# Performance work log

Hardware: AMD Instinct MI355X
Metric: run time of the kernel (lower is better)

The kernel has to match this reference:

```python
import jax, jax.numpy as jnp
import numpy as np

FRONT, END = 1, 2            # COMBINE_FRONT / COMBINE_END label values
BOS_ID, EOS_ID = 0, 1
BS, SLEN, D, H, L = 16, 256, 1024, 16, 2
N_POS = 512                  # N_MAX_POSITIONS


def setup_inputs():
    key = jax.random.key(0)
    ks = iter(jax.random.split(key, 80))
    nrm = lambda shape: jax.random.normal(next(ks), shape, dtype=jnp.float32) * 0.02
    inp = {}
    inp["encoded"] = jax.random.normal(next(ks), (BS, SLEN, D), dtype=jnp.float32)
    inp["lengths"] = jnp.full((BS,), SLEN, dtype=jnp.int32)  # assert slen == lengths.max()
    # deterministic valid word-span labels: [F,F,F,E,O,F,E,O] repeated -> words of 4 and 2 subwords
    pat = np.tile(np.array([1, 1, 1, 2, 0, 1, 2, 0], dtype=np.int32), SLEN // 8)
    inp["combine_labels"] = jnp.asarray(np.broadcast_to(pat, (BS, SLEN)).copy())
    inp["lang_id"] = 0
    inp["pos_emb"] = nrm((N_POS, D))
    inp["special_emb"] = nrm((3, D)).at[2].set(0.0)  # padding_idx=2 row zeroed
    for p in ("ctx", "wc"):
        for w in ("Wq", "Wk", "Wv", "Wo"):
            inp[p + "_" + w] = nrm((L, D, D))
        for b in ("bq", "bk", "bv", "bo", "b2", "be1", "be2"):
            inp[p + "_" + b] = jnp.zeros((L, D), dtype=jnp.float32)
        inp[p + "_W1"] = nrm((L, D, 4 * D))
        inp[p + "_b1"] = jnp.zeros((L, 4 * D), dtype=jnp.float32)
        inp[p + "_W2"] = nrm((L, 4 * D, D))
        inp[p + "_g1"] = jnp.ones((L, D), dtype=jnp.float32)
        inp[p + "_g2"] = jnp.ones((L, D), dtype=jnp.float32)
    return inp


def _ln(x, g, b):
    m = x.mean(-1, keepdims=True)
    v = ((x - m) ** 2).mean(-1, keepdims=True)
    return (x - m) / jnp.sqrt(v + 1e-5) * g + b


def _encoder(x, pad, P):
    # post-norm TransformerEncoder (torch default): attn -> add&LN -> relu-FFN -> add&LN
    Wq, Wk, Wv, Wo, bq, bk, bv, bo, W1, b1, W2, b2, g1, be1, g2, be2 = P
    B, S, Dm = x.shape
    hd = Dm // H
    scale = 1.0 / np.sqrt(hd)
    for i in range(Wq.shape[0]):
        q = (x @ Wq[i] + bq[i]).reshape(B, S, H, hd)
        k = (x @ Wk[i] + bk[i]).reshape(B, S, H, hd)
        v = (x @ Wv[i] + bv[i]).reshape(B, S, H, hd)
        s = jnp.einsum("bqhd,bkhd->bhqk", q, k) * scale
        s = jnp.where(pad[:, None, None, :], -1e9, s)  # src_key_padding_mask
        a = jax.nn.softmax(s, axis=-1)
        o = jnp.einsum("bhqk,bkhd->bqhd", a, v).reshape(B, S, Dm) @ Wo[i] + bo[i]
        x = _ln(x + o, g1[i], be1[i])
        h = jax.nn.relu(x @ W1[i] + b1[i]) @ W2[i] + b2[i]
        x = _ln(x + h, g2[i], be2[i])
    return x


def _word_inputs(encoded, combine_labels, special_emb):
    # vectorized replacement of the nested python-loop ragged span builder;
    # index math on the (concrete) labels in numpy, gathers/scatters in jnp.
    cl = np.asarray(combine_labels)
    f = cl == FRONT
    e = cl == END
    c = np.cumsum(f.astype(np.int64), axis=1)
    frontrun = c - np.maximum.accumulate(np.where(f, 0, c), axis=1)  # run of FRONTs ending here
    fr_prev = np.pad(frontrun[:, :-1], ((0, 0), (1, 0)))
    slot = np.where(f, frontrun, fr_prev + 1)  # 1-based slot inside word (slot 0 = BOS)
    e_flat = e.reshape(-1)
    wid = np.cumsum(e_flat) - e_flat  # word id = #ENDs strictly before, row-major order
    tok_idx = np.nonzero((f | e).reshape(-1))[0]
    w_tok = wid[tok_idx]
    s_tok = slot.reshape(-1)[tok_idx]
    wlen = fr_prev[e] + 3  # k subwords (fr_prev+1) + BOS + EOS
    n_word = wlen.shape[0]
    maxL = int(wlen.max())
    Dm = encoded.shape[-1]
    x = jnp.zeros((n_word, maxL, Dm), dtype=encoded.dtype)
    x = x.at[:, 0].set(special_emb[BOS_ID])
    x = x.at[np.arange(n_word), wlen - 1].set(special_emb[EOS_ID])  # eos at slot k+1
    x = x.at[w_tok, s_tok].set(encoded.reshape(-1, Dm)[tok_idx])
    return x, wlen


def _forward(encoded, lengths, combine_labels, pos_emb, special_emb, ctx, wc):
    S = encoded.shape[1]
    pad = jnp.asarray(np.arange(S)[None, :] >= np.asarray(lengths)[:, None])
    x = _encoder(encoded + pos_emb[:S][None], pad, ctx)          # another_encode
    winp, wlen = _word_inputs(x, combine_labels, special_emb)    # ragged gather, [n_word, maxL, D]
    maxL = winp.shape[1]
    wpad = jnp.asarray(np.arange(maxL)[None, :] >= wlen[:, None])
    y = _encoder(winp + pos_emb[:maxL][None], wpad, wc)          # word_encode
    return y[:, 0]  # position-0 (BOS) representation, [n_word, D]


def reference(encoded, lengths, combine_labels, lang_id, pos_emb, special_emb,
              ctx_Wq, ctx_Wk, ctx_Wv, ctx_Wo, ctx_bq, ctx_bk, ctx_bv, ctx_bo,
              ctx_W1, ctx_b1, ctx_W2, ctx_b2, ctx_g1, ctx_be1, ctx_g2, ctx_be2,
              wc_Wq, wc_Wk, wc_Wv, wc_Wo, wc_bq, wc_bk, wc_bv, wc_bo,
              wc_W1, wc_b1, wc_W2, wc_b2, wc_g1, wc_be1, wc_g2, wc_be2):
    ctx = (ctx_Wq, ctx_Wk, ctx_Wv, ctx_Wo, ctx_bq, ctx_bk, ctx_bv, ctx_bo,
           ctx_W1, ctx_b1, ctx_W2, ctx_b2, ctx_g1, ctx_be1, ctx_g2, ctx_be2)
    wc = (wc_Wq, wc_Wk, wc_Wv, wc_Wo, wc_bq, wc_bk, wc_bv, wc_bo,
          wc_W1, wc_b1, wc_W2, wc_b2, wc_g1, wc_be1, wc_g2, wc_be2)
    return _forward(encoded, lengths, combine_labels, pos_emb, special_emb, ctx, wc)
```

## Files before the change

kernel.cpp:

```cpp
#include <hip/hip_runtime.h>
#include <stdint.h>

typedef unsigned short u16;
typedef __attribute__((ext_vector_type(8))) short short8;
typedef __attribute__((ext_vector_type(4))) short short4v;
typedef __attribute__((ext_vector_type(4))) float f32x4;

#define DEV static __device__ __forceinline__

constexpr int B = 16, S = 256, D = 1024, H = 16, LYR = 2, FF = 4096;
constexpr int Mc = B * S;
constexpr int MAXL = 6;
constexpr int QKVS = 3 * D;

DEV u16 f2b(float f) {
  union { float f; uint32_t u; } a; a.f = f;
  uint32_t r = a.u + 0x7fffu + ((a.u >> 16) & 1u);
  return (u16)(r >> 16);
}
DEV float b2f(u16 b) {
  union { uint32_t u; float f; } a; a.u = ((uint32_t)b) << 16;
  return a.f;
}

DEV void glds16(const u16* g, u16* l) {
  __builtin_amdgcn_global_load_lds((const __attribute__((address_space(1))) void*)g,
                                   (__attribute__((address_space(3))) void*)l, 16, 0, 0);
}

struct TBatch {
  const float* src[6];
  u16* dst[6];
  int Kd[6];
  int Nd[6];
  int base[6];
};

__global__ __launch_bounds__(256) void transpose_batch(TBatch tb, int unused) {
  __shared__ float tile[64][65];
  const int bid = blockIdx.x;
  int wi = 0;
#pragma unroll
  for (int i = 1; i < 6; i++)
    if (bid >= tb.base[i]) wi = i;
  const float* __restrict__ W = tb.src[wi];
  u16* __restrict__ Wt = tb.dst[wi];
  const int K = tb.Kd[wi], N = tb.Nd[wi];
  const int local = bid - tb.base[wi];
  const int ntx = N >> 6;
  const int bn = (local % ntx) * 64, bk = (local / ntx) * 64;
  const int t = threadIdx.x;
  const int lr = t >> 2, lc = (t & 3) * 16;
#pragma unroll
  for (int q = 0; q < 4; q++) {
    float4 v = *(const float4*)&W[(size_t)(bk + lr) * N + bn + lc + q * 4];
    *(float4*)&tile[lr][lc + q * 4] = v;
  }
  __syncthreads();
  const int k0 = (t & 7) * 8;
#pragma unroll
  for (int p = 0; p < 2; p++) {
    const int n = (t >> 3) + p * 32;
    short8 o;
#pragma unroll
    for (int j = 0; j < 8; j++) o[j] = (short)f2b(tile[k0 + j][n]);
    *(short8*)&Wt[(size_t)(bn + n) * K + bk + k0] = o;
  }
}


template <int PASSES>
DEV void stage_rows(const u16* P, int lda, int k0, u16* Dst, int t) {
#pragma unroll
  for (int p = 0; p < PASSES; p++)
    glds16(P + (size_t)(p * 32) * lda + k0, Dst + p * 2048 + t * 8);
}

DEV void compute_tile(const u16* Asb, const u16* Bsb, f32x4 (&acc)[4][8],
                      int wm, int wn, int li, int hi) {
#pragma unroll
  for (int ks = 0; ks < 2; ks++) {
    const int ch = ((((ks << 2) | hi) ^ (li & 7)) * 8);
    short8 af[4], bfr[8];
#pragma unroll
    for (int i = 0; i < 4; i++)
      af[i] = *(const short8*)&Asb[(wm + i * 16 + li) * 64 + ch];
#pragma unroll
    for (int j = 0; j < 8; j++)
      bfr[j] = *(const short8*)&Bsb[(wn + j * 16 + li) * 64 + ch];
#pragma unroll
    for (int i = 0; i < 4; i++)
#pragma unroll
      for (int j = 0; j < 8; j++)
        acc[i][j] = __builtin_amdgcn_mfma_f32_16x16x32_bf16(af[i], bfr[j], acc[i][j], 0, 0, 0);
  }
}

template <int EPI, bool SPLITB, bool SPLITK>
__global__ __launch_bounds__(256, 2) void gemm_bt(const u16* __restrict__ A,
                                                  const u16* __restrict__ Bt,
                                                  const float* __restrict__ bias0,
                                                  const float* __restrict__ bias1,
                                                  const float* __restrict__ bias2,
                                                  float* __restrict__ Cf, u16* __restrict__ Cb,
                                                  int M, int N, int K, int lda, int NB) {
  __shared__ u16 As[128 * 64];
  __shared__ u16 Bs[256 * 64];
  const int t = threadIdx.x, lane = t & 63, w = t >> 6;
  const int wm = (w >> 1) * 64, wn = (w & 1) * 128;
  const int nwg = gridDim.x;
  const int cpx = nwg >> 3;
  const int swz = (blockIdx.x & 7) * cpx + (blockIdx.x >> 3);
  int sblk = 0, rem = swz;
  if (SPLITK) {
    const int tps = nwg >> 1;
    sblk = (swz >= tps) ? 1 : 0;
    rem = swz - sblk * tps;
  }
  const int n0 = (rem % NB) * 256, m0 = (rem / NB) * 128;
  const int pr = t >> 3;
  const int scb = (((t & 7) ^ (pr & 7)) * 8);
  f32x4 acc[4][8] = {};
  const u16* Ap = A + (size_t)sblk * K + (size_t)(m0 + pr) * lda + scb;
  const u16* Bp = Bt + (size_t)sblk * K + (size_t)(n0 + pr) * lda + scb;
  const int li = lane & 15, hi = lane >> 4;

  for (int k0 = 0; k0 < K; k0 += 64) {
    stage_rows<4>(Ap, lda, k0, &As[0], t);
    stage_rows<8>(Bp, lda, k0, &Bs[0], t);
    __syncthreads();
    compute_tile(&As[0], &Bs[0], acc, wm, wn, li, hi);
    __syncthreads();
  }

  u16* Cbs = Cb;
  if (SPLITK && EPI == 3) Cbs = Cb + (size_t)sblk * M * N;
  const int rg = hi * 4;
#pragma unroll
  for (int j = 0; j < 8; j++) {
    const int col = n0 + wn + j * 16 + li;
    float bv = 0.f;
    if (EPI != 3)
      bv = SPLITB ? (col < 1024 ? bias0 : col < 2048 ? bias1 : bias2)[col & 1023]
                  : bias0[col];
#pragma unroll
    for (int i = 0; i < 4; i++) {
      const int row0 = m0 + wm + i * 16 + rg;
#pragma unroll
      for (int r = 0; r < 4; r++) {
        float v = acc[i][j][r] + bv;
        if (EPI == 2) v = fmaxf(v, 0.f);
        if (EPI == 0) Cf[(size_t)(row0 + r) * N + col] = v;
        else Cbs[(size_t)(row0 + r) * N + col] = f2b(v);
      }
    }
  }
}

__global__ __launch_bounds__(256) void transpose_v(const u16* __restrict__ QKV,
                                                   u16* __restrict__ Vt) {
  const int kb = blockIdx.x, h = blockIdx.y, b = blockIdx.z;
  __shared__ u16 tile[64][72];
  const int t = threadIdx.x, lr = t >> 3, lc = (t & 7) * 8;
#pragma unroll
  for (int p = 0; p < 2; p++) {
    int r = lr + p * 32;
    *(short8*)&tile[r][lc] =
        *(const short8*)&QKV[(size_t)(b * 256 + kb * 64 + r) * QKVS + 2048 + h * 64 + lc];
  }
  __syncthreads();
#pragma unroll
  for (int p = 0; p < 2; p++) {
    int hd = lr + p * 32;
    short8 v8;
#pragma unroll
    for (int j = 0; j < 8; j++) v8[j] = (short)tile[lc + j][hd];
    *(short8*)&Vt[(size_t)((b * 16 + h) * 64 + hd) * 256 + kb * 64 + lc] = v8;
  }
}

__global__ __launch_bounds__(256) void attn_ctx(const u16* __restrict__ QKV,
                                                const u16* __restrict__ Vt,
                                                u16* __restrict__ AO,
                                                const int* __restrict__ lengths) {
  const int qt = blockIdx.x, h = blockIdx.y, b = blockIdx.z;
  __shared__ u16 Qs[64 * 64], Ks[64 * 64], Vs[64 * 64], Ps[64 * 64];
  const int t = threadIdx.x, lane = t & 63, w = t >> 6;
  const int len = lengths[b];
  const bool full = (len >= 256);
  const int lr = t >> 3, lc = (t & 7) * 8;
#pragma unroll
  for (int p = 0; p < 2; p++) {
    int r = lr + p * 32;
    *(short8*)&Qs[r * 64 + lc] =
        *(const short8*)&QKV[(size_t)(b * 256 + qt * 64 + r) * QKVS + h * 64 + lc];
  }
  const int li = lane & 15, kk = (lane >> 4) * 8, rg = (lane >> 4) * 4;
  float mrun[4], lrun[4];
  f32x4 oacc[4] = {};
#pragma unroll
  for (int r = 0; r < 4; r++) { mrun[r] = -1e30f; lrun[r] = 0.f; }

  for (int kt = 0; kt < 4; kt++) {
    __syncthreads();
#pragma unroll
    for (int p = 0; p < 2; p++) {
      int r = lr + p * 32;
      *(short8*)&Ks[r * 64 + lc] =
          *(const short8*)&QKV[(size_t)(b * 256 + kt * 64 + r) * QKVS + 1024 + h * 64 + lc];
      *(short8*)&Vs[r * 64 + lc] =
          *(const short8*)&Vt[(size_t)((b * 16 + h) * 64 + r) * 256 + kt * 64 + lc];
    }
    __syncthreads();
    f32x4 s[4] = {};
    short8 aq0 = *(const short8*)&Qs[(w * 16 + li) * 64 + kk];
    short8 aq1 = *(const short8*)&Qs[(w * 16 + li) * 64 + 32 + kk];
    __builtin_amdgcn_s_setprio(1);
#pragma unroll
    for (int fn = 0; fn < 4; fn++) {
      short8 b0 = *(const short8*)&Ks[(fn * 16 + li) * 64 + kk];
      short8 b1 = *(const short8*)&Ks[(fn * 16 + li) * 64 + 32 + kk];
      s[fn] = __builtin_amdgcn_mfma_f32_16x16x32_bf16(aq0, b0, s[fn], 0, 0, 0);
      s[fn] = __builtin_amdgcn_mfma_f32_16x16x32_bf16(aq1, b1, s[fn], 0, 0, 0);
    }
    __builtin_amdgcn_s_setprio(0);
    float pv[4][4];
    if (full) {
#pragma unroll
      for (int r = 0; r < 4; r++) {
        float mx = -1e30f;
#pragma unroll
        for (int fn = 0; fn < 4; fn++) {
          float v = s[fn][r] * 0.125f;
          pv[fn][r] = v;
          mx = fmaxf(mx, v);
        }
#pragma unroll
        for (int d = 1; d < 16; d <<= 1) mx = fmaxf(mx, __shfl_xor(mx, d));
        if (mx > mrun[r] + 8.f) {
          float sf = __expf(mrun[r] - mx);
          mrun[r] = mx;
          lrun[r] *= sf;
#pragma unroll
          for (int fn = 0; fn < 4; fn++) oacc[fn][r] *= sf;
        }
        float rs = 0.f;
#pragma unroll
        for (int fn = 0; fn < 4; fn++) {
          float p = __expf(pv[fn][r] - mrun[r]);
          pv[fn][r] = p;
          rs += p;
        }
#pragma unroll
        for (int d = 1; d < 16; d <<= 1) rs += __shfl_xor(rs, d);
        lrun[r] += rs;
      }
    } else {
#pragma unroll
      for (int r = 0; r < 4; r++) {
        float mx = -1e30f;
#pragma unroll
        for (int fn = 0; fn < 4; fn++) {
          int key = kt * 64 + fn * 16 + li;
          float v = (key < len) ? s[fn][r] * 0.125f : -1e30f;
          pv[fn][r] = v;
          mx = fmaxf(mx, v);
        }
#pragma unroll
        for (int d = 1; d < 16; d <<= 1) mx = fmaxf(mx, __shfl_xor(mx, d));
        float mnew = fmaxf(mrun[r], mx);
        float sf = __expf(mrun[r] - mnew);
        mrun[r] = mnew;
        float rs = 0.f;
#pragma unroll
        for (int fn = 0; fn < 4; fn++) {
          int key = kt * 64 + fn * 16 + li;
          float p = (key < len) ? __expf(pv[fn][r] - mnew) : 0.f;
          pv[fn][r] = p;
          rs += p;
        }
#pragma unroll
        for (int d = 1; d < 16; d <<= 1) rs += __shfl_xor(rs, d);
        lrun[r] = lrun[r] * sf + rs;
#pragma unroll
        for (int fn = 0; fn < 4; fn++) oacc[fn][r] *= sf;
      }
    }
#pragma unroll
    for (int fn = 0; fn < 4; fn++)
#pragma unroll
      for (int r = 0; r < 4; r++)
        Ps[(w * 16 + rg + r) * 64 + fn * 16 + li] = f2b(pv[fn][r]);
    __builtin_amdgcn_s_setprio(1);
#pragma unroll
    for (int ks = 0; ks < 2; ks++) {
      short8 ap = *(const short8*)&Ps[(w * 16 + li) * 64 + ks * 32 + kk];
#pragma unroll
      for (int fn = 0; fn < 4; fn++) {
        short8 bv = *(const short8*)&Vs[(fn * 16 + li) * 64 + ks * 32 + kk];
        oacc[fn] = __builtin_amdgcn_mfma_f32_16x16x32_bf16(ap, bv, oacc[fn], 0, 0, 0);
      }
    }
    __builtin_amdgcn_s_setprio(0);
  }
#pragma unroll
  for (int r = 0; r < 4; r++) {
    float inv = 1.f / fmaxf(lrun[r], 1e-30f);
    int row = b * 256 + qt * 64 + w * 16 + rg + r;
#pragma unroll
    for (int fn = 0; fn < 4; fn++) {
      int col = h * 64 + fn * 16 + li;
      AO[(size_t)row * 1024 + col] = f2b(oacc[fn][r] * inv);
    }
  }
}

__global__ __launch_bounds__(256) void attn_word(const u16* __restrict__ QKV,
                                                 const int* __restrict__ wlen,
                                                 u16* __restrict__ AO, int NW) {
  const int idx = blockIdx.x * 256 + threadIdx.x;
  if (idx >= NW * 16 * MAXL) return;
  const int i = idx % MAXL, h = (idx / MAXL) % 16, wd = idx / (MAXL * 16);
  const int len = wlen[wd];
  const size_t rowb = (size_t)(wd * MAXL + i) * QKVS;
  float q[64];
#pragma unroll
  for (int d = 0; d < 64; d += 8) {
    short8 q8 = *(const short8*)&QKV[rowb + h * 64 + d];
#pragma unroll
    for (int e = 0; e < 8; e++) q[d + e] = b2f((u16)q8[e]);
  }
  float sc[MAXL];
  float mx = -1e30f;
  for (int j = 0; j < MAXL; j++) {
    if (j >= len) { sc[j] = -1e30f; continue; }
    const size_t koff = (size_t)(wd * MAXL + j) * QKVS + 1024 + h * 64;
    float dot = 0.f;
#pragma unroll
    for (int d = 0; d < 64; d += 8) {
      short8 k8 = *(const short8*)&QKV[koff + d];
#pragma unroll
      for (int e = 0; e < 8; e++) dot += q[d + e] * b2f((u16)k8[e]);
    }
    sc[j] = dot * 0.125f;
    mx = fmaxf(mx, sc[j]);
  }
  float p[MAXL], l = 0.f;
  for (int j = 0; j < MAXL; j++) {
    p[j] = (j < len) ? __expf(sc[j] - mx) : 0.f;
    l += p[j];
  }
  const float rl = 1.f / fmaxf(l, 1e-30f);
  for (int j = 0; j < MAXL; j++) p[j] *= rl;
#pragma unroll
  for (int d = 0; d < 64; d += 8) {
    float acc[8] = {};
    for (int j = 0; j < MAXL; j++) {
      if (j >= len) break;
      short8 v8 = *(const short8*)&QKV[(size_t)(wd * MAXL + j) * QKVS + 2048 + h * 64 + d];
#pragma unroll
      for (int e = 0; e < 8; e++) acc[e] += p[j] * b2f((u16)v8[e]);
    }
    short8 o8;
#pragma unroll
    for (int e = 0; e < 8; e++) o8[e] = (short)f2b(acc[e]);
    *(short8*)&AO[(size_t)(wd * MAXL + i) * 1024 + h * 64 + d] = o8;
  }
}

__global__ __launch_bounds__(256) void ln_resid2(const float* __restrict__ X,
                                                 const u16* __restrict__ P0,
                                                 const u16* __restrict__ P1,
                                                 const float* __restrict__ bias,
                                                 const float* __restrict__ g,
                                                 const float* __restrict__ be,
                                                 float* __restrict__ Xo, u16* __restrict__ Xb) {
  const int row = blockIdx.x, t = threadIdx.x;
  const size_t base = (size_t)row * 1024 + t * 4;
  float4 x4 = *(const float4*)&X[base];
  short4v p0 = *(const short4v*)&P0[base];
  short4v p1 = *(const short4v*)&P1[base];
  float4 bb = *(const float4*)&bias[t * 4];
  float v[4];
  v[0] = x4.x + b2f((u16)p0[0]) + b2f((u16)p1[0]) + bb.x;
  v[1] = x4.y + b2f((u16)p0[1]) + b2f((u16)p1[1]) + bb.y;
  v[2] = x4.z + b2f((u16)p0[2]) + b2f((u16)p1[2]) + bb.z;
  v[3] = x4.w + b2f((u16)p0[3]) + b2f((u16)p1[3]) + bb.w;
  float s = v[0] + v[1] + v[2] + v[3];
  float q = v[0] * v[0] + v[1] * v[1] + v[2] * v[2] + v[3] * v[3];
#pragma unroll
  for (int d = 1; d < 64; d <<= 1) { s += __shfl_xor(s, d); q += __shfl_xor(q, d); }
  __shared__ float ss[4], qq[4];
  if ((t & 63) == 0) { ss[t >> 6] = s; qq[t >> 6] = q; }
  __syncthreads();
  s = ss[0] + ss[1] + ss[2] + ss[3];
  q = qq[0] + qq[1] + qq[2] + qq[3];
  const float mean = s * (1.f / 1024.f);
  const float var = q * (1.f / 1024.f) - mean * mean;
  const float rstd = rsqrtf(var + 1e-5f);
  float4 gv = *(const float4*)&g[t * 4];
  float4 bv = *(const float4*)&be[t * 4];
  float y[4];
  y[0] = (v[0] - mean) * rstd * gv.x + bv.x;
  y[1] = (v[1] - mean) * rstd * gv.y + bv.y;
  y[2] = (v[2] - mean) * rstd * gv.z + bv.z;
  y[3] = (v[3] - mean) * rstd * gv.w + bv.w;
  *(float4*)&Xo[base] = make_float4(y[0], y[1], y[2], y[3]);
  short4v o = { (short)f2b(y[0]), (short)f2b(y[1]), (short)f2b(y[2]), (short)f2b(y[3]) };
  *(short4v*)&Xb[base] = o;
}

__global__ __launch_bounds__(256) void posadd(const float* __restrict__ enc,
                                              const float* __restrict__ pos,
                                              float* __restrict__ X, u16* __restrict__ Xb) {
  const int row = blockIdx.x, t = threadIdx.x;
  const int sp = row & 255;
  const size_t base = (size_t)row * 1024 + t * 4;
  float4 e = *(const float4*)&enc[base];
  float4 p = *(const float4*)&pos[(size_t)sp * 1024 + t * 4];
  float y[4] = { e.x + p.x, e.y + p.y, e.z + p.z, e.w + p.w };
  *(float4*)&X[base] = make_float4(y[0], y[1], y[2], y[3]);
  short4v o = { (short)f2b(y[0]), (short)f2b(y[1]), (short)f2b(y[2]), (short)f2b(y[3]) };
  *(short4v*)&Xb[base] = o;
}

__global__ void scan_words(const int* __restrict__ labels, int* __restrict__ t2w,
                           int* __restrict__ t2s, int* __restrict__ wlen) {
  __shared__ int rowEnds[16], rowBase[16];
  const int t = threadIdx.x;
  if (t < 16) {
    int c = 0;
    for (int s = 0; s < 256; s++) c += (labels[t * 256 + s] == 2);
    rowEnds[t] = c;
  }
  __syncthreads();
  if (t == 0) {
    int acc = 0;
    for (int b2 = 0; b2 < 16; b2++) { rowBase[b2] = acc; acc += rowEnds[b2]; }
  }
  __syncthreads();
  if (t < 16) {
    int wc = rowBase[t], fr = 0;
    for (int s = 0; s < 256; s++) {
      const int tok = t * 256 + s, lb = labels[tok];
      if (lb == 1) { fr++; t2w[tok] = wc; t2s[tok] = fr; }
      else if (lb == 2) { t2w[tok] = wc; t2s[tok] = fr + 1; wlen[wc] = fr + 3; wc++; fr = 0; }
      else { t2w[tok] = -1; t2s[tok] = 0; fr = 0; }
    }
  }
}

__global__ __launch_bounds__(256) void build_winp(const float* __restrict__ pos,
                                                  const float* __restrict__ spec,
                                                  const int* __restrict__ wlen,
                                                  float* __restrict__ XW) {
  const int row = blockIdx.x;
  const int wd = row / MAXL, sl = row % MAXL;
  const int len = wlen[wd];
  const int t = threadIdx.x;
  const size_t cb = t * 4;
  float4 p = *(const float4*)&pos[(size_t)sl * 1024 + cb];
  float4 e = make_float4(0.f, 0.f, 0.f, 0.f);
  if (sl == 0) e = *(const float4*)&spec[cb];
  else if (sl == len - 1) e = *(const float4*)&spec[1024 + cb];
  *(float4*)&XW[(size_t)row * 1024 + cb] =
      make_float4(p.x + e.x, p.y + e.y, p.z + e.z, p.w + e.w);
}

__global__ __launch_bounds__(256) void scatter_tokens(const float* __restrict__ Xc,
                                                      const int* __restrict__ t2w,
                                                      const int* __restrict__ t2s,
                                                      float* __restrict__ XW) {
  const int tok = blockIdx.x;
  const int wd = t2w[tok];
  if (wd < 0) return;
  const int row = wd * MAXL + t2s[tok];
  const size_t cb = threadIdx.x * 4;
  float4 a = *(const float4*)&Xc[(size_t)tok * 1024 + cb];
  float* dst = &XW[(size_t)row * 1024 + cb];
  float4 b2 = *(const float4*)dst;
  *(float4*)dst = make_float4(a.x + b2.x, a.y + b2.y, a.z + b2.z, a.w + b2.w);
}

__global__ __launch_bounds__(256) void to_bf16_k(const float* __restrict__ X,
                                                 u16* __restrict__ Xb) {
  const size_t base = (size_t)blockIdx.x * 1024 + threadIdx.x * 4;
  float4 v = *(const float4*)&X[base];
  short4v o = { (short)f2b(v.x), (short)f2b(v.y), (short)f2b(v.z), (short)f2b(v.w) };
  *(short4v*)&Xb[base] = o;
}

__global__ __launch_bounds__(256) void gather_out(const float* __restrict__ XW,
                                                  float* __restrict__ out) {
  const int wd = blockIdx.x;
  const size_t cb = threadIdx.x * 4;
  *(float4*)&out[(size_t)wd * 1024 + cb] =
      *(const float4*)&XW[(size_t)(wd * MAXL) * 1024 + cb];
}

extern "C" void kernel_launch(void* const* d_in, const int* in_sizes, int n_in,
                              void* d_out, int out_size, void* d_ws, size_t ws_size,
                              hipStream_t stream) {
  const float* encoded = (const float*)d_in[0];
  const int* lengths = (const int*)d_in[1];
  const int* labels = (const int*)d_in[2];
  const float* pos = (const float*)d_in[4];
  const float* spec = (const float*)d_in[5];
  const float* W[2][16];
  for (int p = 0; p < 2; p++)
    for (int i = 0; i < 16; i++) W[p][i] = (const float*)d_in[6 + p * 16 + i];

  const int NW = out_size / D;
  const int Mw = NW * MAXL;

  char* wp = (char*)d_ws;
  size_t off = 0;
  auto alloc = [&](size_t bytes) {
    void* r = wp + off;
    off += (bytes + 255) & ~(size_t)255;
    return r;
  };
  float* x_ctx = (float*)alloc((size_t)Mc * D * 4);
  float* x_word = (float*)alloc((size_t)Mw * D * 4);
  u16* xb = (u16*)alloc((size_t)Mw * D * 2);
  u16* wtQKV = (u16*)alloc((size_t)3 * D * D * 2);
  u16* wtO = (u16*)alloc((size_t)D * D * 2);
  u16* wtW1 = (u16*)alloc((size_t)D * FF * 2);
  u16* wtW2 = (u16*)alloc((size_t)D * FF * 2);
  char* uni = (char*)alloc((size_t)Mw * FF * 2);
  u16* QKV = (u16*)uni;
  u16* Vt = (u16*)(uni + ((size_t)40 << 20));
  u16* hb = (u16*)uni;
  u16* AOb = (u16*)alloc((size_t)Mw * D * 2);
  u16* tmpb = (u16*)alloc((size_t)2 * Mw * D * 2);
  int* t2w = (int*)alloc((size_t)Mc * 4);
  int* t2s = (int*)alloc((size_t)Mc * 4);
  int* wlen = (int*)alloc((size_t)NW * 4);
  (void)ws_size; (void)in_sizes; (void)n_in;

  posadd<<<Mc, 256, 0, stream>>>(encoded, pos, x_ctx, xb);

  auto run_encoder = [&](int p, float* X, int M, bool is_ctx) {
    for (int l = 0; l < LYR; l++) {
      const size_t oDD = (size_t)l * D * D, oDF = (size_t)l * D * FF;
      TBatch tb;
      tb.src[0] = W[p][0] + oDD; tb.dst[0] = wtQKV;               tb.Kd[0] = D;  tb.Nd[0] = D;
      tb.src[1] = W[p][1] + oDD; tb.dst[1] = wtQKV + (size_t)D * D;   tb.Kd[1] = D;  tb.Nd[1] = D;
      tb.src[2] = W[p][2] + oDD; tb.dst[2] = wtQKV + (size_t)2 * D * D; tb.Kd[2] = D; tb.Nd[2] = D;
      tb.src[3] = W[p][3] + oDD; tb.dst[3] = wtO;                 tb.Kd[3] = D;  tb.Nd[3] = D;
      tb.src[4] = W[p][11] + oDF; tb.dst[4] = wtW1;               tb.Kd[4] = D;  tb.Nd[4] = FF;
      tb.src[5] = W[p][13] + oDF; tb.dst[5] = wtW2;               tb.Kd[5] = FF; tb.Nd[5] = D;
      int base = 0;
      for (int i = 0; i < 6; i++) {
        tb.base[i] = base;
        base += (tb.Kd[i] / 64) * (tb.Nd[i] / 64);
      }
      transpose_batch<<<base, 256, 0, stream>>>(tb, 0);

      gemm_bt<1, true, false><<<(3 * D / 256) * (M / 128), 256, 0, stream>>>(
          xb, wtQKV, W[p][4] + (size_t)l * D, W[p][5] + (size_t)l * D,
          W[p][6] + (size_t)l * D, nullptr, QKV, M, 3 * D, D, D, 3 * D / 256);
      if (is_ctx) {
        transpose_v<<<dim3(4, H, B), 256, 0, stream>>>(QKV, Vt);
        attn_ctx<<<dim3(4, H, B), 256, 0, stream>>>(QKV, Vt, AOb, lengths);
      } else {
        attn_word<<<(NW * H * MAXL + 255) / 256, 256, 0, stream>>>(QKV, wlen, AOb, NW);
      }
      gemm_bt<3, false, true><<<2 * (D / 256) * (M / 128), 256, 0, stream>>>(
          AOb, wtO, nullptr, nullptr, nullptr, nullptr, tmpb, M, D, 512, D, D / 256);
      ln_resid2<<<M, 256, 0, stream>>>(X, tmpb, tmpb + (size_t)M * D, W[p][7] + (size_t)l * D,
                                       W[p][14] + (size_t)l * D, W[p][9] + (size_t)l * D, X, xb);
      gemm_bt<2, false, false><<<(FF / 256) * (M / 128), 256, 0, stream>>>(
          xb, wtW1, W[p][12] + (size_t)l * FF, nullptr, nullptr, nullptr, hb, M, FF, D, D,
          FF / 256);
      gemm_bt<3, false, true><<<2 * (D / 256) * (M / 128), 256, 0, stream>>>(
          hb, wtW2, nullptr, nullptr, nullptr, nullptr, tmpb, M, D, 2048, FF, D / 256);
      ln_resid2<<<M, 256, 0, stream>>>(X, tmpb, tmpb + (size_t)M * D, W[p][8] + (size_t)l * D,
                                       W[p][15] + (size_t)l * D, W[p][10] + (size_t)l * D, X, xb);
    }
  };

  run_encoder(0, x_ctx, Mc, true);

  scan_words<<<1, 64, 0, stream>>>(labels, t2w, t2s, wlen);
  build_winp<<<Mw, 256, 0, stream>>>(pos, spec, wlen, x_word);
  scatter_tokens<<<Mc, 256, 0, stream>>>(x_ctx, t2w, t2s, x_word);
  to_bf16_k<<<Mw, 256, 0, stream>>>(x_word, xb);

  run_encoder(1, x_word, Mw, false);

  gather_out<<<NW, 256, 0, stream>>>(x_word, (float*)d_out);
}
```

Measured before the change: 1.013 ms.

## Use double-buffered 256x256 GEMM with 4-way split-K for FFN and output projections

Adds a new GEMM kernel for the O-projection, W1 and W2 matmuls. It uses 512 threads, 256x256 output tiles and two LDS buffers, so the global-to-LDS loads for the next K slice are issued while the current slice is being computed. MFMA issue is wrapped in s_setprio. The O-projection and W2 now split K four ways instead of two, and a new LayerNorm-residual kernel sums four bf16 partials. The QKV GEMM keeps the old kernel, now specialised. The larger tiles and about 128KB of LDS allow one block per CU, and the extra split-K partials add more bf16 traffic and rounding in exchange for better load/compute overlap.

```diff
diff --git a/kernel.cpp b/kernel.cpp
--- a/kernel.cpp
+++ b/kernel.cpp
@@ -7,6 +7,7 @@
 typedef __attribute__((ext_vector_type(4))) float f32x4;
 
 #define DEV static __device__ __forceinline__
+#define WAITVM(N) asm volatile("s_waitcnt vmcnt(" #N ")" ::: "memory")
 
 constexpr int B = 16, S = 256, D = 1024, H = 16, LYR = 2, FF = 4096;
 constexpr int Mc = B * S;
@@ -68,7 +69,6 @@
   }
 }
 
-
 template <int PASSES>
 DEV void stage_rows(const u16* P, int lda, int k0, u16* Dst, int t) {
 #pragma unroll
@@ -96,14 +96,13 @@
   }
 }
 
-template <int EPI, bool SPLITB, bool SPLITK>
-__global__ __launch_bounds__(256, 2) void gemm_bt(const u16* __restrict__ A,
-                                                  const u16* __restrict__ Bt,
-                                                  const float* __restrict__ bias0,
-                                                  const float* __restrict__ bias1,
-                                                  const float* __restrict__ bias2,
-                                                  float* __restrict__ Cf, u16* __restrict__ Cb,
-                                                  int M, int N, int K, int lda, int NB) {
+__global__ __launch_bounds__(256, 2) void gemm_qkv(const u16* __restrict__ A,
+                                                   const u16* __restrict__ Bt,
+                                                   const float* __restrict__ bias0,
+                                                   const float* __restrict__ bias1,
+                                                   const float* __restrict__ bias2,
+                                                   u16* __restrict__ Cb,
+                                                   int M, int N, int K, int lda, int NB) {
   __shared__ u16 As[128 * 64];
   __shared__ u16 Bs[256 * 64];
   const int t = threadIdx.x, lane = t & 63, w = t >> 6;
@@ -111,18 +110,12 @@
   const int nwg = gridDim.x;
   const int cpx = nwg >> 3;
   const int swz = (blockIdx.x & 7) * cpx + (blockIdx.x >> 3);
-  int sblk = 0, rem = swz;
-  if (SPLITK) {
-    const int tps = nwg >> 1;
-    sblk = (swz >= tps) ? 1 : 0;
-    rem = swz - sblk * tps;
-  }
-  const int n0 = (rem % NB) * 256, m0 = (rem / NB) * 128;
+  const int n0 = (swz % NB) * 256, m0 = (swz / NB) * 128;
   const int pr = t >> 3;
   const int scb = (((t & 7) ^ (pr & 7)) * 8);
   f32x4 acc[4][8] = {};
-  const u16* Ap = A + (size_t)sblk * K + (size_t)(m0 + pr) * lda + scb;
-  const u16* Bp = Bt + (size_t)sblk * K + (size_t)(n0 + pr) * lda + scb;
+  const u16* Ap = A + (size_t)(m0 + pr) * lda + scb;
+  const u16* Bp = Bt + (size_t)(n0 + pr) * lda + scb;
   const int li = lane & 15, hi = lane >> 4;
 
   for (int k0 = 0; k0 < K; k0 += 64) {
@@ -133,25 +126,130 @@
     __syncthreads();
   }
 
-  u16* Cbs = Cb;
-  if (SPLITK && EPI == 3) Cbs = Cb + (size_t)sblk * M * N;
   const int rg = hi * 4;
 #pragma unroll
   for (int j = 0; j < 8; j++) {
     const int col = n0 + wn + j * 16 + li;
+    const float bv = (col < 1024 ? bias0 : col < 2048 ? bias1 : bias2)[col & 1023];
+#pragma unroll
+    for (int i = 0; i < 4; i++) {
+      const int row0 = m0 + wm + i * 16 + rg;
+#pragma unroll
+      for (int r = 0; r < 4; r++)
+        Cb[(size_t)(row0 + r) * N + col] = f2b(acc[i][j][r] + bv);
+    }
+  }
+}
+
+
+template <int PASSES>
+DEV void stage_rows2(const u16* P, int lda, int k0, u16* Dst, int t) {
+#pragma unroll
+  for (int p = 0; p < PASSES; p++)
+    glds16(P + (size_t)(p * 64) * lda + k0, Dst + p * 4096 + t * 8);
+}
+
+DEV void compute_tile2(const u16* Asb, const u16* Bsb, f32x4 (&acc)[8][4],
+                       int wm, int wn, int li, int hi) {
+#pragma unroll
+  for (int ks = 0; ks < 2; ks++) {
+    const int ch = ((((ks << 2) | hi) ^ (li & 7)) * 8);
+    short8 af[8], bfr[4];
+#pragma unroll
+    for (int i = 0; i < 8; i++)
+      af[i] = *(const short8*)&Asb[(wm + i * 16 + li) * 64 + ch];
+#pragma unroll
+    for (int j = 0; j < 4; j++)
+      bfr[j] = *(const short8*)&Bsb[(wn + j * 16 + li) * 64 + ch];
+    __builtin_amdgcn_s_setprio(1);
+#pragma unroll
+    for (int i = 0; i < 8; i++)
+#pragma unroll
+      for (int j = 0; j < 4; j++)
+        acc[i][j] = __builtin_amdgcn_mfma_f32_16x16x32_bf16(af[i], bfr[j], acc[i][j], 0, 0, 0);
+    __builtin_amdgcn_s_setprio(0);
+  }
+}
+
+template <int EPI, int SPLITK>
+__global__ __launch_bounds__(512, 1) void gemm_bt2(const u16* __restrict__ A,
+                                                   const u16* __restrict__ Bt,
+                                                   const float* __restrict__ bias0,
+                                                   u16* __restrict__ Cb,
+                                                   int M, int N, int K, int lda, int NB) {
+  __shared__ u16 As[2][256 * 64];
+  __shared__ u16 Bs[2][256 * 64];
+  const int t = threadIdx.x, lane = t & 63, w = t >> 6;
+  const int wm = (w >> 2) * 128, wn = (w & 3) * 64;
+  const int nwg = gridDim.x;
+  const int cpx = nwg >> 3;
+  const int swz = ((int)blockIdx.x & 7) * cpx + ((int)blockIdx.x >> 3);
+  int sblk = 0, rem = swz;
+  if (SPLITK > 0) {
+    const int tps = nwg / SPLITK;
+    sblk = swz / tps;
+    rem = swz % tps;
+  }
+  const int n0 = (rem % NB) * 256, m0 = (rem / NB) * 256;
+  const int pr = t >> 3;
+  const int scb = (((t & 7) ^ (pr & 7)) * 8);
+  f32x4 acc[8][4] = {};
+  const u16* Ap = A + (size_t)sblk * K + (size_t)(m0 + pr) * lda + scb;
+  const u16* Bp = Bt + (size_t)sblk * K + (size_t)(n0 + pr) * lda + scb;
+  const int li = lane & 15, hi = lane >> 4;
+
+  const int nt = K >> 6;
+  stage_rows2<4>(Ap, lda, 0, &As[0][0], t);
+  stage_rows2<4>(Bp, lda, 0, &Bs[0][0], t);
+  stage_rows2<4>(Ap, lda, 64, &As[1][0], t);
+  stage_rows2<4>(Bp, lda, 64, &Bs[1][0], t);
+  WAITVM(8);
+  __builtin_amdgcn_s_barrier();
+  __builtin_amdgcn_sched_barrier(0);
+
+  for (int kt = 0; kt < nt; kt += 2) {
+    compute_tile2(&As[0][0], &Bs[0][0], acc, wm, wn, li, hi);
+    __builtin_amdgcn_s_barrier();
+    __builtin_amdgcn_sched_barrier(0);
+    if (kt + 2 < nt) {
+      stage_rows2<4>(Ap, lda, (kt + 2) << 6, &As[0][0], t);
+      stage_rows2<4>(Bp, lda, (kt + 2) << 6, &Bs[0][0], t);
+      WAITVM(8);
+    } else {
+      WAITVM(0);
+    }
+    __builtin_amdgcn_s_barrier();
+    __builtin_amdgcn_sched_barrier(0);
+    compute_tile2(&As[1][0], &Bs[1][0], acc, wm, wn, li, hi);
+    __builtin_amdgcn_s_barrier();
+    __builtin_amdgcn_sched_barrier(0);
+    if (kt + 3 < nt) {
+      stage_rows2<4>(Ap, lda, (kt + 3) << 6, &As[1][0], t);
+      stage_rows2<4>(Bp, lda, (kt + 3) << 6, &Bs[1][0], t);
+      WAITVM(8);
+    } else {
+      WAITVM(0);
+    }
+    __builtin_amdgcn_s_barrier();
+    __builtin_amdgcn_sched_barrier(0);
+  }
+
+  u16* Cbs = Cb;
+  if (SPLITK > 0 && EPI == 3) Cbs = Cb + (size_t)sblk * M * N;
+  const int rg = hi * 4;
+#pragma unroll
+  for (int j = 0; j < 4; j++) {
+    const int col = n0 + wn + j * 16 + li;
     float bv = 0.f;
-    if (EPI != 3)
-      bv = SPLITB ? (col < 1024 ? bias0 : col < 2048 ? bias1 : bias2)[col & 1023]
-                  : bias0[col];
-#pragma unroll
-    for (int i = 0; i < 4; i++) {
+    if (EPI != 3) bv = bias0[col];
+#pragma unroll
+    for (int i = 0; i < 8; i++) {
       const int row0 = m0 + wm + i * 16 + rg;
 #pragma unroll
       for (int r = 0; r < 4; r++) {
         float v = acc[i][j][r] + bv;
         if (EPI == 2) v = fmaxf(v, 0.f);
-        if (EPI == 0) Cf[(size_t)(row0 + r) * N + col] = v;
-        else Cbs[(size_t)(row0 + r) * N + col] = f2b(v);
+        Cbs[(size_t)(row0 + r) * N + col] = f2b(v);
       }
     }
   }
@@ -368,9 +466,9 @@
   }
 }
 
-__global__ __launch_bounds__(256) void ln_resid2(const float* __restrict__ X,
-                                                 const u16* __restrict__ P0,
-                                                 const u16* __restrict__ P1,
+__global__ __launch_bounds__(256) void ln_resid4(const float* __restrict__ X,
+                                                 const u16* __restrict__ P,
+                                                 size_t pstride,
                                                  const float* __restrict__ bias,
                                                  const float* __restrict__ g,
                                                  const float* __restrict__ be,
@@ -378,14 +476,16 @@
   const int row = blockIdx.x, t = threadIdx.x;
   const size_t base = (size_t)row * 1024 + t * 4;
   float4 x4 = *(const float4*)&X[base];
-  short4v p0 = *(const short4v*)&P0[base];
-  short4v p1 = *(const short4v*)&P1[base];
   float4 bb = *(const float4*)&bias[t * 4];
-  float v[4];
-  v[0] = x4.x + b2f((u16)p0[0]) + b2f((u16)p1[0]) + bb.x;
-  v[1] = x4.y + b2f((u16)p0[1]) + b2f((u16)p1[1]) + bb.y;
-  v[2] = x4.z + b2f((u16)p0[2]) + b2f((u16)p1[2]) + bb.z;
-  v[3] = x4.w + b2f((u16)p0[3]) + b2f((u16)p1[3]) + bb.w;
+  float v[4] = { x4.x + bb.x, x4.y + bb.y, x4.z + bb.z, x4.w + bb.w };
+#pragma unroll
+  for (int k = 0; k < 4; k++) {
+    short4v pk = *(const short4v*)&P[base + k * pstride];
+    v[0] += b2f((u16)pk[0]);
+    v[1] += b2f((u16)pk[1]);
+    v[2] += b2f((u16)pk[2]);
+    v[3] += b2f((u16)pk[3]);
+  }
   float s = v[0] + v[1] + v[2] + v[3];
   float q = v[0] * v[0] + v[1] * v[1] + v[2] * v[2] + v[3] * v[3];
 #pragma unroll
@@ -532,7 +632,7 @@
   u16* Vt = (u16*)(uni + ((size_t)40 << 20));
   u16* hb = (u16*)uni;
   u16* AOb = (u16*)alloc((size_t)Mw * D * 2);
-  u16* tmpb = (u16*)alloc((size_t)2 * Mw * D * 2);
+  u16* tmpb = (u16*)alloc((size_t)4 * Mw * D * 2);
   int* t2w = (int*)alloc((size_t)Mc * 4);
   int* t2s = (int*)alloc((size_t)Mc * 4);
   int* wlen = (int*)alloc((size_t)NW * 4);
@@ -557,25 +657,24 @@
       }
       transpose_batch<<<base, 256, 0, stream>>>(tb, 0);
 
-      gemm_bt<1, true, false><<<(3 * D / 256) * (M / 128), 256, 0, stream>>>(
+      gemm_qkv<<<(3 * D / 256) * (M / 128), 256, 0, stream>>>(
           xb, wtQKV, W[p][4] + (size_t)l * D, W[p][5] + (size_t)l * D,
-          W[p][6] + (size_t)l * D, nullptr, QKV, M, 3 * D, D, D, 3 * D / 256);
+          W[p][6] + (size_t)l * D, QKV, M, 3 * D, D, D, 3 * D / 256);
       if (is_ctx) {
         transpose_v<<<dim3(4, H, B), 256, 0, stream>>>(QKV, Vt);
         attn_ctx<<<dim3(4, H, B), 256, 0, stream>>>(QKV, Vt, AOb, lengths);
       } else {
         attn_word<<<(NW * H * MAXL + 255) / 256, 256, 0, stream>>>(QKV, wlen, AOb, NW);
       }
-      gemm_bt<3, false, true><<<2 * (D / 256) * (M / 128), 256, 0, stream>>>(
-          AOb, wtO, nullptr, nullptr, nullptr, nullptr, tmpb, M, D, 512, D, D / 256);
-      ln_resid2<<<M, 256, 0, stream>>>(X, tmpb, tmpb + (size_t)M * D, W[p][7] + (size_t)l * D,
+      gemm_bt2<3, 4><<<4 * (D / 256) * (M / 256), 512, 0, stream>>>(
+          AOb, wtO, nullptr, tmpb, M, D, 256, D, D / 256);
+      ln_resid4<<<M, 256, 0, stream>>>(X, tmpb, (size_t)M * D, W[p][7] + (size_t)l * D,
                                        W[p][14] + (size_t)l * D, W[p][9] + (size_t)l * D, X, xb);
-      gemm_bt<2, false, false><<<(FF / 256) * (M / 128), 256, 0, stream>>>(
-          xb, wtW1, W[p][12] + (size_t)l * FF, nullptr, nullptr, nullptr, hb, M, FF, D, D,
-          FF / 256);
-      gemm_bt<3, false, true><<<2 * (D / 256) * (M / 128), 256, 0, stream>>>(
-          hb, wtW2, nullptr, nullptr, nullptr, nullptr, tmpb, M, D, 2048, FF, D / 256);
-      ln_resid2<<<M, 256, 0, stream>>>(X, tmpb, tmpb + (size_t)M * D, W[p][8] + (size_t)l * D,
+      gemm_bt2<2, 0><<<(FF / 256) * (M / 256), 512, 0, stream>>>(
+          xb, wtW1, W[p][12] + (size_t)l * FF, hb, M, FF, D, D, FF / 256);
+      gemm_bt2<3, 4><<<4 * (D / 256) * (M / 256), 512, 0, stream>>>(
+          hb, wtW2, nullptr, tmpb, M, D, 1024, FF, D / 256);
+      ln_resid4<<<M, 256, 0, stream>>>(X, tmpb, (size_t)M * D, W[p][8] + (size_t)l * D,
                                        W[p][15] + (size_t)l * D, W[p][10] + (size_t)l * D, X, xb);
     }
   };
```

New measurement: 1.127 ms. +11.3%, slower.
